# Performance work log

Hardware: AMD Instinct MI355X
Metric: run time of the kernel (lower is better)

Reference implementation:

```python
import jax, jax.numpy as jnp
import numpy as np

N = 100000
E = 1600000
IN = 256
H = 4
D = 32           # n_hidden per head
C = 47           # n_classes per head in last layer
NEG_SLOPE = 0.2


def setup_inputs() -> dict:
    key = jax.random.key(0)
    ks = jax.random.split(key, 20)
    x = jax.random.normal(ks[0], (N, IN), dtype=jnp.float32)
    src = jax.random.randint(ks[1], (E,), 0, N, dtype=jnp.int32)
    dst = jax.random.randint(ks[2], (E,), 0, N, dtype=jnp.int32)
    s = 0.05
    inp = {"x": x, "src": src, "dst": dst}
    # layer 0: in 256 -> (H=4, D=32)
    inp["W0s"] = jax.random.normal(ks[3], (IN, H * D), dtype=jnp.float32) * s
    inp["W0d"] = jax.random.normal(ks[4], (IN, H * D), dtype=jnp.float32) * s
    inp["a0l"] = jax.random.normal(ks[5], (H, D), dtype=jnp.float32) * s
    inp["a0r"] = jax.random.normal(ks[6], (H, D), dtype=jnp.float32) * s
    inp["b0"] = jnp.zeros((H, D), dtype=jnp.float32)
    # layer 1: in 128 -> (4, 32)
    inp["W1s"] = jax.random.normal(ks[7], (H * D, H * D), dtype=jnp.float32) * s
    inp["W1d"] = jax.random.normal(ks[8], (H * D, H * D), dtype=jnp.float32) * s
    inp["a1l"] = jax.random.normal(ks[9], (H, D), dtype=jnp.float32) * s
    inp["a1r"] = jax.random.normal(ks[10], (H, D), dtype=jnp.float32) * s
    inp["b1"] = jnp.zeros((H, D), dtype=jnp.float32)
    # layer 2: in 128 -> (4, 47), no activation
    inp["W2s"] = jax.random.normal(ks[11], (H * D, H * C), dtype=jnp.float32) * s
    inp["W2d"] = jax.random.normal(ks[12], (H * D, H * C), dtype=jnp.float32) * s
    inp["a2l"] = jax.random.normal(ks[13], (H, C), dtype=jnp.float32) * s
    inp["a2r"] = jax.random.normal(ks[14], (H, C), dtype=jnp.float32) * s
    inp["b2"] = jnp.zeros((H, C), dtype=jnp.float32)
    return inp


def _gat_layer(h, src, dst, Ws, Wd, al, ar, b):
    # h: [N, F_in]; full-graph block so h_dst == h
    n = h.shape[0]
    heads, dout = al.shape
    fs = (h @ Ws).reshape(n, heads, dout)   # [N, H, D]
    fd = (h @ Wd).reshape(n, heads, dout)
    el = jnp.sum(fs * al, axis=-1)          # [N, H]
    er = jnp.sum(fd * ar, axis=-1)
    e = el[src] + er[dst]                   # [E, H]
    e = jnp.where(e > 0, e, NEG_SLOPE * e)  # leaky_relu
    # segment softmax over incoming edges of each dst node
    m = jax.lax.stop_gradient(jax.ops.segment_max(e, dst, num_segments=n))
    ez = jnp.exp(e - m[dst])
    denom = jax.ops.segment_sum(ez, dst, num_segments=n)
    alpha = ez / denom[dst]                 # [E, H]
    msg = fs[src] * alpha[:, :, None]       # [E, H, D]
    rst = jax.ops.segment_sum(msg, dst, num_segments=n)  # [N, H, D]
    return rst + b


def reference(x, src, dst,
              W0s, W0d, a0l, a0r, b0,
              W1s, W1d, a1l, a1r, b1,
              W2s, W2d, a2l, a2r, b2):
    h = _gat_layer(x, src, dst, W0s, W0d, a0l, a0r, b0)
    h = jax.nn.relu(h).reshape(h.shape[0], -1)           # flatten(1)
    h = _gat_layer(h, src, dst, W1s, W1d, a1l, a1r, b1)
    h = jax.nn.relu(h).reshape(h.shape[0], -1)
    h = _gat_layer(h, src, dst, W2s, W2d, a2l, a2r, b2)  # [N, H, C]
    h = h.mean(axis=1)                                   # mean over heads
    return jax.nn.log_softmax(h, axis=-1)
```

## Files before the change

kernel.cpp:

```cpp
#include <hip/hip_runtime.h>
#include <math.h>

#define NEG_SLOPE 0.2f

typedef _Float16 half2v __attribute__((ext_vector_type(2)));
typedef _Float16 half8 __attribute__((ext_vector_type(8)));
typedef float float4v __attribute__((ext_vector_type(4)));
typedef float float2v __attribute__((ext_vector_type(2)));

__device__ __forceinline__ float lrelu(float x) { return x > 0.f ? x : NEG_SLOPE * x; }

__device__ __forceinline__ float sel4(const float4 v, int h) {
  float r = v.x;
  r = (h == 1) ? v.y : r;
  r = (h == 2) ? v.z : r;
  r = (h == 3) ? v.w : r;
  return r;
}

__device__ __forceinline__ unsigned char f32_to_fp8(float a) {
  int v = __builtin_amdgcn_cvt_pk_fp8_f32(a, 0.f, 0, false);
  return (unsigned char)(v & 0xff);
}


__global__ void k_hist(const int* __restrict__ dst, int* __restrict__ cnt, int E) {
  int i = blockIdx.x * blockDim.x + threadIdx.x;
  if (i < E) atomicAdd(&cnt[dst[i]], 1);
}

__global__ __launch_bounds__(256) void k_offsets(const int* __restrict__ cnt,
                                                 int* __restrict__ row_start,
                                                 int* __restrict__ gcount, int N) {
  __shared__ int s[256];
  __shared__ int base;
  int tid = threadIdx.x;
  int i = blockIdx.x * 256 + tid;
  int c = (i < N) ? cnt[i] : 0;
  s[tid] = c;
  __syncthreads();
  for (int off = 1; off < 256; off <<= 1) {
    int v = 0;
    if (tid >= off) v = s[tid - off];
    __syncthreads();
    if (tid >= off) s[tid] += v;
    __syncthreads();
  }
  if (tid == 255) base = atomicAdd(gcount, s[255]);
  __syncthreads();
  if (i < N) row_start[i] = base + s[tid] - c;
}

__global__ void k_scatter(const int* __restrict__ src, const int* __restrict__ dst,
                          const int* __restrict__ row_start, int* __restrict__ fill,
                          int* __restrict__ srcs, int E) {
  int i = blockIdx.x * blockDim.x + threadIdx.x;
  if (i < E) {
    int d = dst[i];
    int p = row_start[d] + atomicAdd(&fill[d], 1);
    srcs[p] = src[i];
  }
}

__device__ __forceinline__ void wlr_one(const float* Ws, const float* Wd,
                                        const float* al, const float* ar,
                                        float* wlr, int K, int Dh, int i) {
  int M = 4 * Dh;
  int k = i >> 2, h = i & 3;
  float sl = 0.f, sr = 0.f;
  for (int d = 0; d < Dh; d++) {
    sl += Ws[(size_t)k * M + h * Dh + d] * al[h * Dh + d];
    sr += Wd[(size_t)k * M + h * Dh + d] * ar[h * Dh + d];
  }
  wlr[k * 8 + h] = sl;
  wlr[k * 8 + 4 + h] = sr;
}

__global__ __launch_bounds__(256) void k_prep(
    const float* __restrict__ W0s, const float* __restrict__ W0d,
    const float* __restrict__ a0l, const float* __restrict__ a0r,
    const float* __restrict__ W1s, const float* __restrict__ W1d,
    const float* __restrict__ a1l, const float* __restrict__ a1r,
    const float* __restrict__ W2s, const float* __restrict__ W2d,
    const float* __restrict__ a2l, const float* __restrict__ a2r,
    float* __restrict__ wlr0, float* __restrict__ wlr1, float* __restrict__ wlr2,
    _Float16* __restrict__ Wt0, _Float16* __restrict__ Wt1, _Float16* __restrict__ Wt2) {
  int i = blockIdx.x * 256 + threadIdx.x;
  if (i < 1024) {
    wlr_one(W0s, W0d, a0l, a0r, wlr0, 256, 32, i);
  } else if (i < 1536) {
    wlr_one(W1s, W1d, a1l, a1r, wlr1, 128, 32, i - 1024);
  } else if (i < 2048) {
    wlr_one(W2s, W2d, a2l, a2r, wlr2, 128, 47, i - 1536);
  } else if (i < 2048 + 32768) {
    int j = i - 2048;
    int m = j >> 8, k = j & 255;
    Wt0[j] = (_Float16)W0s[(size_t)k * 128 + m];
  } else if (i < 2048 + 32768 + 16384) {
    int j = i - (2048 + 32768);
    int m = j >> 7, k = j & 127;
    Wt1[j] = (_Float16)W1s[(size_t)k * 128 + m];
  } else if (i < 2048 + 32768 + 16384 + 24576) {
    int j = i - (2048 + 32768 + 16384);
    int r = j >> 7, k = j & 127;
    int h = r / 48, c = r % 48;
    float v = (c < 47) ? W2s[(size_t)k * 188 + 47 * h + c] : 0.f;
    Wt2[j] = (_Float16)v;
  }
}

template <int BN, typename AT>
__global__ __launch_bounds__(256) void k_gemm_mfma(const AT* __restrict__ A,
                                                   const _Float16* __restrict__ Bt,
                                                   const float* __restrict__ wlr,
                                                   unsigned char* __restrict__ C,
                                                   float* __restrict__ el,
                                                   float* __restrict__ er, int N, int K) {
  constexpr int NT = BN / 64;
  constexpr int ASZ = 4 * 64 * 8;
  constexpr int BSZ = (BN / 16) * 64 * 8;
  constexpr int SSZ = ASZ + BSZ;
  __shared__ __align__(16) _Float16 smem[SSZ];
  __shared__ float swlr[2048];
  _Float16* As = smem;
  _Float16* Bs = smem + ASZ;

  const int tid = threadIdx.x;
  const int lane = tid & 63;
  const int w = tid >> 6;
  const int row0 = blockIdx.x * 64;

  for (int i = tid; i < K * 8; i += 256) swlr[i] = wlr[i];
  __syncthreads();

  float4v acc[4][NT];
#pragma unroll
  for (int i = 0; i < 4; i++)
#pragma unroll
    for (int j = 0; j < NT; j++) acc[i][j] = (float4v){0.f, 0.f, 0.f, 0.f};
  float p[8] = {0, 0, 0, 0, 0, 0, 0, 0};

  const int ar_ = tid >> 2, aq = tid & 3;
  for (int k0 = 0; k0 < K; k0 += 32) {
    {
      int gr = row0 + ar_;
      float a8[8];
      if (gr < N) {
        if constexpr (sizeof(AT) == 4) {
          const float4* pp = (const float4*)&A[(size_t)gr * K + k0 + aq * 8];
          float4 u0 = pp[0], u1 = pp[1];
          a8[0] = u0.x; a8[1] = u0.y; a8[2] = u0.z; a8[3] = u0.w;
          a8[4] = u1.x; a8[5] = u1.y; a8[6] = u1.z; a8[7] = u1.w;
        } else {
          half8 hv = *(const half8*)&A[(size_t)gr * K + k0 + aq * 8];
#pragma unroll
          for (int j = 0; j < 8; j++) a8[j] = (float)hv[j];
        }
      } else {
#pragma unroll
        for (int j = 0; j < 8; j++) a8[j] = 0.f;
      }
      half8 v;
#pragma unroll
      for (int j = 0; j < 8; j++) v[j] = (_Float16)a8[j];
      *(half8*)&As[(size_t)(((ar_ >> 4) * 64) + (ar_ & 15) + 16 * aq) * 8] = v;
#pragma unroll
      for (int j = 0; j < 8; j++) {
        const float av = a8[j];
        const float* wp = &swlr[(k0 + aq * 8 + j) * 8];
        float4 w0 = *(const float4*)wp;
        float4 w1 = *(const float4*)(wp + 4);
        p[0] += av * w0.x; p[1] += av * w0.y; p[2] += av * w0.z; p[3] += av * w0.w;
        p[4] += av * w1.x; p[5] += av * w1.y; p[6] += av * w1.z; p[7] += av * w1.w;
      }
    }
#pragma unroll
    for (int i = 0; i < NT; i++) {
      int idx = tid + i * 256;
      int n = idx >> 2, q = idx & 3;
      half8 v = *(const half8*)&Bt[(size_t)n * K + k0 + q * 8];
      *(half8*)&Bs[(size_t)((n >> 4) * 64 + (n & 15) + 16 * q) * 8] = v;
    }
    __syncthreads();
    half8 af[4];
#pragma unroll
    for (int mt = 0; mt < 4; mt++) af[mt] = *(half8*)&As[(size_t)(mt * 64 + lane) * 8];
#pragma unroll
    for (int nt = 0; nt < NT; nt++) {
      half8 bf = *(half8*)&Bs[(size_t)((w * NT + nt) * 64 + lane) * 8];
#pragma unroll
      for (int mt = 0; mt < 4; mt++)
        acc[mt][nt] = __builtin_amdgcn_mfma_f32_16x16x32_f16(af[mt], bf, acc[mt][nt], 0, 0, 0);
    }
    __syncthreads();
  }

#pragma unroll
  for (int j = 0; j < 8; j++) swlr[(ar_ * 4 + aq) * 8 + j] = p[j];

  unsigned char* cs = (unsigned char*)smem;
  const int quad = lane >> 4;
#pragma unroll
  for (int mt = 0; mt < 4; mt++)
#pragma unroll
    for (int nt = 0; nt < NT; nt++)
#pragma unroll
      for (int reg = 0; reg < 4; reg++) {
        int r = mt * 16 + quad * 4 + reg;
        int cc = (w * NT + nt) * 16 + (lane & 15);
        cs[r * BN + cc] = f32_to_fp8(acc[mt][nt][reg]);
      }
  __syncthreads();
  if (tid < 64) {
    int gr = row0 + tid;
    if (gr < N) {
      float e[8];
#pragma unroll
      for (int j = 0; j < 8; j++)
        e[j] = swlr[(tid * 4 + 0) * 8 + j] + swlr[(tid * 4 + 1) * 8 + j] +
               swlr[(tid * 4 + 2) * 8 + j] + swlr[(tid * 4 + 3) * 8 + j];
      *(float4*)&el[(size_t)gr * 4] = make_float4(e[0], e[1], e[2], e[3]);
      *(float4*)&er[(size_t)gr * 4] = make_float4(e[4], e[5], e[6], e[7]);
    }
  }
  constexpr int PER = (64 * BN) / (256 * 16);
  const uint4* s4 = (const uint4*)cs;
#pragma unroll
  for (int i = 0; i < PER; i++) {
    int idx = tid + i * 256;
    int r = idx / (BN / 16), c16 = idx % (BN / 16);
    int gr = row0 + r;
    if (gr < N) *(uint4*)&C[(size_t)gr * BN + c16 * 16] = s4[idx];
  }
}

__global__ __launch_bounds__(256) void k_edge_mid(
    const unsigned char* __restrict__ F, const float* __restrict__ el,
    const float* __restrict__ er, const int* __restrict__ row_start,
    const int* __restrict__ cnt, const int* __restrict__ srcs,
    const float* __restrict__ bias, _Float16* __restrict__ hout, int N) {
  __shared__ float sEz[4][64][4];
  __shared__ int sU[4][64];
  int lane = threadIdx.x & 63;
  int w = threadIdx.x >> 6;
  int v = blockIdx.x * 4 + w;
  if (v >= N) return;
  int start = row_start[v], deg = cnt[v];
  float4 erv = *(const float4*)&er[(size_t)v * 4];
  const int g = lane >> 4;
  const int fl = lane & 15;
  const int h = fl >> 2;
  float acc[8] = {0, 0, 0, 0, 0, 0, 0, 0};
  float4 lsum = make_float4(0.f, 0.f, 0.f, 0.f);

  for (int c = 0; c < deg; c += 64) {
    int take = min(64, deg - c);
    if (lane < take) {
      int u = srcs[start + c + lane];
      float4 e = *(const float4*)&el[(size_t)u * 4];
      float4 ez;
      ez.x = __expf(lrelu(e.x + erv.x));
      ez.y = __expf(lrelu(e.y + erv.y));
      ez.z = __expf(lrelu(e.z + erv.z));
      ez.w = __expf(lrelu(e.w + erv.w));
      lsum.x += ez.x; lsum.y += ez.y; lsum.z += ez.z; lsum.w += ez.w;
      sU[w][lane] = u;
      *(float4*)&sEz[w][lane][0] = ez;
    }
    for (int kk = g; kk < take; kk += 4) {
      int u = sU[w][kk];
      float ezh = sEz[w][kk][h];
      uint2 d = *(const uint2*)&F[(size_t)u * 128 + 8 * fl];
      float2v c0 = __builtin_amdgcn_cvt_pk_f32_fp8((int)d.x, false);
      float2v c1 = __builtin_amdgcn_cvt_pk_f32_fp8((int)d.x, true);
      float2v c2 = __builtin_amdgcn_cvt_pk_f32_fp8((int)d.y, false);
      float2v c3 = __builtin_amdgcn_cvt_pk_f32_fp8((int)d.y, true);
      acc[0] += ezh * c0.x; acc[1] += ezh * c0.y;
      acc[2] += ezh * c1.x; acc[3] += ezh * c1.y;
      acc[4] += ezh * c2.x; acc[5] += ezh * c2.y;
      acc[6] += ezh * c3.x; acc[7] += ezh * c3.y;
    }
  }
#pragma unroll
  for (int j = 0; j < 8; j++) {
    acc[j] += __shfl_xor(acc[j], 16);
    acc[j] += __shfl_xor(acc[j], 32);
  }
#pragma unroll
  for (int msk = 1; msk < 64; msk <<= 1) {
    lsum.x += __shfl_xor(lsum.x, msk);
    lsum.y += __shfl_xor(lsum.y, msk);
    lsum.z += __shfl_xor(lsum.z, msk);
    lsum.w += __shfl_xor(lsum.w, msk);
  }
  if (g == 0) {
    float inv = (deg > 0) ? 1.f / sel4(lsum, h) : 0.f;
    const float4* bp = (const float4*)&bias[8 * fl];
    float4 b0v = bp[0], b1v = bp[1];
    float bb[8] = {b0v.x, b0v.y, b0v.z, b0v.w, b1v.x, b1v.y, b1v.z, b1v.w};
    half8 o;
#pragma unroll
    for (int j = 0; j < 8; j++) o[j] = (_Float16)fmaxf(fmaf(acc[j], inv, bb[j]), 0.f);
    *(half8*)&hout[(size_t)v * 128 + 8 * fl] = o;
  }
}

__global__ __launch_bounds__(256) void k_edge_final(
    const unsigned char* __restrict__ F, const float* __restrict__ el,
    const float* __restrict__ er, const int* __restrict__ row_start,
    const int* __restrict__ cnt, const int* __restrict__ srcs,
    const float* __restrict__ b2, float* __restrict__ out, int N) {
  __shared__ float sEz[4][64][4];
  __shared__ int sU[4][64];
  __shared__ float red[4][192];
  int lane = threadIdx.x & 63;
  int w = threadIdx.x >> 6;
  int v = blockIdx.x * 4 + w;
  if (v >= N) return;
  int start = row_start[v], deg = cnt[v];
  float4 erv = *(const float4*)&er[(size_t)v * 4];
  const int sub = lane >> 5;
  const int l24 = lane & 31;
  const bool act = l24 < 24;
  const int h = l24 / 6;
  const int j6 = l24 % 6;
  const int foff = 48 * h + 8 * j6;
  float acc[8] = {0, 0, 0, 0, 0, 0, 0, 0};
  float4 lsum = make_float4(0.f, 0.f, 0.f, 0.f);

  for (int c = 0; c < deg; c += 64) {
    int take = min(64, deg - c);
    if (lane < take) {
      int u = srcs[start + c + lane];
      float4 e = *(const float4*)&el[(size_t)u * 4];
      float4 ez;
      ez.x = __expf(lrelu(e.x + erv.x));
      ez.y = __expf(lrelu(e.y + erv.y));
      ez.z = __expf(lrelu(e.z + erv.z));
      ez.w = __expf(lrelu(e.w + erv.w));
      lsum.x += ez.x; lsum.y += ez.y; lsum.z += ez.z; lsum.w += ez.w;
      sU[w][lane] = u;
      *(float4*)&sEz[w][lane][0] = ez;
    }
    if (act) {
      for (int kk = sub; kk < take; kk += 2) {
        int u = sU[w][kk];
        float ezh = sEz[w][kk][h];
        uint2 d = *(const uint2*)&F[(size_t)u * 192 + foff];
        float2v c0 = __builtin_amdgcn_cvt_pk_f32_fp8((int)d.x, false);
        float2v c1 = __builtin_amdgcn_cvt_pk_f32_fp8((int)d.x, true);
        float2v c2 = __builtin_amdgcn_cvt_pk_f32_fp8((int)d.y, false);
        float2v c3 = __builtin_amdgcn_cvt_pk_f32_fp8((int)d.y, true);
        acc[0] += ezh * c0.x; acc[1] += ezh * c0.y;
        acc[2] += ezh * c1.x; acc[3] += ezh * c1.y;
        acc[4] += ezh * c2.x; acc[5] += ezh * c2.y;
        acc[6] += ezh * c3.x; acc[7] += ezh * c3.y;
      }
    }
  }
#pragma unroll
  for (int j = 0; j < 8; j++) acc[j] += __shfl_xor(acc[j], 32);
#pragma unroll
  for (int msk = 1; msk < 64; msk <<= 1) {
    lsum.x += __shfl_xor(lsum.x, msk);
    lsum.y += __shfl_xor(lsum.y, msk);
    lsum.z += __shfl_xor(lsum.z, msk);
    lsum.w += __shfl_xor(lsum.w, msk);
  }
  if (act && sub == 0) {
    float inv = (deg > 0) ? 1.f / sel4(lsum, h) : 0.f;
#pragma unroll
    for (int j = 0; j < 8; j++) {
      int cc = 8 * j6 + j;
      float bv = (cc < 47) ? b2[47 * h + cc] : 0.f;
      red[w][foff + j] = fmaf(acc[j], inv, bv);
    }
  }
  __syncthreads();
  float g = -INFINITY;
  if (lane < 47)
    g = 0.25f * (red[w][lane] + red[w][lane + 48] + red[w][lane + 96] + red[w][lane + 144]);
  float gm = g;
#pragma unroll
  for (int msk = 1; msk < 64; msk <<= 1) gm = fmaxf(gm, __shfl_xor(gm, msk));
  float ex = (lane < 47) ? __expf(g - gm) : 0.f;
  float s = ex;
#pragma unroll
  for (int msk = 1; msk < 64; msk <<= 1) s += __shfl_xor(s, msk);
  if (lane < 47) out[(size_t)v * 47 + lane] = g - gm - __logf(s);
}

extern "C" void kernel_launch(void* const* d_in, const int* in_sizes, int n_in,
                              void* d_out, int out_size, void* d_ws, size_t ws_size,
                              hipStream_t stream) {
  const float* x = (const float*)d_in[0];
  const int* src = (const int*)d_in[1];
  const int* dst = (const int*)d_in[2];
  const float* W0s = (const float*)d_in[3];
  const float* W0d = (const float*)d_in[4];
  const float* a0l = (const float*)d_in[5];
  const float* a0r = (const float*)d_in[6];
  const float* b0 = (const float*)d_in[7];
  const float* W1s = (const float*)d_in[8];
  const float* W1d = (const float*)d_in[9];
  const float* a1l = (const float*)d_in[10];
  const float* a1r = (const float*)d_in[11];
  const float* b1 = (const float*)d_in[12];
  const float* W2s = (const float*)d_in[13];
  const float* W2d = (const float*)d_in[14];
  const float* a2l = (const float*)d_in[15];
  const float* a2r = (const float*)d_in[16];
  const float* b2 = (const float*)d_in[17];
  float* out = (float*)d_out;

  const int N = in_sizes[0] / 256;
  const int E = in_sizes[1];

  char* w = (char*)d_ws;
  size_t off = 0;
  auto alloc = [&](size_t bytes) -> void* {
    void* p = w + off;
    off += (bytes + 255) & ~(size_t)255;
    return p;
  };
  int* gcount = (int*)alloc(4);
  int* cnt = (int*)alloc((size_t)N * 4);
  int* fill = (int*)alloc((size_t)N * 4);
  size_t zbytes = off;
  int* row_start = (int*)alloc((size_t)N * 4);
  int* srcs = (int*)alloc((size_t)E * 4);
  float* wlr0 = (float*)alloc(256 * 8 * 4);
  float* wlr1 = (float*)alloc(128 * 8 * 4);
  float* wlr2 = (float*)alloc(128 * 8 * 4);
  _Float16* Wt0 = (_Float16*)alloc(128 * 256 * 2);
  _Float16* Wt1 = (_Float16*)alloc(128 * 128 * 2);
  _Float16* Wt2 = (_Float16*)alloc(192 * 128 * 2);
  float* el = (float*)alloc((size_t)N * 4 * 4);
  float* er = (float*)alloc((size_t)N * 4 * 4);
  unsigned char* F = (unsigned char*)alloc((size_t)N * 192);
  _Float16* Ha = (_Float16*)alloc((size_t)N * 128 * 2);
  _Float16* Hc = (_Float16*)alloc((size_t)N * 128 * 2);
  (void)ws_size;

  hipMemsetAsync(d_ws, 0, zbytes, stream);
  k_hist<<<(E + 255) / 256, 256, 0, stream>>>(dst, cnt, E);
  k_offsets<<<(N + 255) / 256, 256, 0, stream>>>(cnt, row_start, gcount, N);
  k_scatter<<<(E + 255) / 256, 256, 0, stream>>>(src, dst, row_start, fill, srcs, E);
  k_prep<<<(75776 + 255) / 256, 256, 0, stream>>>(W0s, W0d, a0l, a0r, W1s, W1d, a1l, a1r,
                                                  W2s, W2d, a2l, a2r, wlr0, wlr1, wlr2,
                                                  Wt0, Wt1, Wt2);

  int gemm_grid = (N + 63) / 64;
  int node_grid = (N + 3) / 4;

  k_gemm_mfma<128, float><<<gemm_grid, 256, 0, stream>>>(x, Wt0, wlr0, F, el, er, N, 256);
  k_edge_mid<<<node_grid, 256, 0, stream>>>(F, el, er, row_start, cnt, srcs, b0, Ha, N);

  k_gemm_mfma<128, _Float16><<<gemm_grid, 256, 0, stream>>>(Ha, Wt1, wlr1, F, el, er, N, 128);
  k_edge_mid<<<node_grid, 256, 0, stream>>>(F, el, er, row_start, cnt, srcs, b1, Hc, N);

  k_gemm_mfma<192, _Float16><<<gemm_grid, 256, 0, stream>>>(Hc, Wt2, wlr2, F, el, er, N, 128);
  k_edge_final<<<node_grid, 256, 0, stream>>>(F, el, er, row_start, cnt, srcs, b2, out, N);
}
```

Before: 680.1 us.

## Split attention-logit and edge-exp computation into separate kernels before aggregation

Removes the el/er dot-product computation from the MFMA GEMM and moves it to a dedicated per-node kernel that rereads the layer input. A new per-edge kernel precomputes exp(leaky_relu(el[src]+er[dst])) into a CSR-ordered buffer, using a new dsts array written during scatter. The aggregation kernels then stream srcs and Ez with software prefetch instead of staging through shared memory, and the final layer uses 16-byte feature loads. This simplifies the GEMM and aggregation loops but adds extra global traffic: the input features are reread and an E×4 float buffer is written and read per layer, plus extra launches.

```diff
diff --git a/kernel.cpp b/kernel.cpp
--- a/kernel.cpp
+++ b/kernel.cpp
@@ -3,24 +3,31 @@
 
 #define NEG_SLOPE 0.2f
 
-typedef _Float16 half2v __attribute__((ext_vector_type(2)));
 typedef _Float16 half8 __attribute__((ext_vector_type(8)));
 typedef float float4v __attribute__((ext_vector_type(4)));
 typedef float float2v __attribute__((ext_vector_type(2)));
 
 __device__ __forceinline__ float lrelu(float x) { return x > 0.f ? x : NEG_SLOPE * x; }
 
-__device__ __forceinline__ float sel4(const float4 v, int h) {
-  float r = v.x;
-  r = (h == 1) ? v.y : r;
-  r = (h == 2) ? v.z : r;
-  r = (h == 3) ? v.w : r;
-  return r;
-}
-
 __device__ __forceinline__ unsigned char f32_to_fp8(float a) {
   int v = __builtin_amdgcn_cvt_pk_fp8_f32(a, 0.f, 0, false);
   return (unsigned char)(v & 0xff);
+}
+
+__device__ __forceinline__ void acc_fp8x8(float* acc, uint2 d, float ez) {
+  float2v c0 = __builtin_amdgcn_cvt_pk_f32_fp8((int)d.x, false);
+  float2v c1 = __builtin_amdgcn_cvt_pk_f32_fp8((int)d.x, true);
+  float2v c2 = __builtin_amdgcn_cvt_pk_f32_fp8((int)d.y, false);
+  float2v c3 = __builtin_amdgcn_cvt_pk_f32_fp8((int)d.y, true);
+  acc[0] += ez * c0.x; acc[1] += ez * c0.y;
+  acc[2] += ez * c1.x; acc[3] += ez * c1.y;
+  acc[4] += ez * c2.x; acc[5] += ez * c2.y;
+  acc[6] += ez * c3.x; acc[7] += ez * c3.y;
+}
+
+__device__ __forceinline__ void acc_fp8x16(float* acc, uint4 d, float ez) {
+  acc_fp8x8(acc, make_uint2(d.x, d.y), ez);
+  acc_fp8x8(acc + 8, make_uint2(d.z, d.w), ez);
 }
 
 
@@ -53,12 +60,13 @@
 
 __global__ void k_scatter(const int* __restrict__ src, const int* __restrict__ dst,
                           const int* __restrict__ row_start, int* __restrict__ fill,
-                          int* __restrict__ srcs, int E) {
+                          int* __restrict__ srcs, int* __restrict__ dsts, int E) {
   int i = blockIdx.x * blockDim.x + threadIdx.x;
   if (i < E) {
     int d = dst[i];
     int p = row_start[d] + atomicAdd(&fill[d], 1);
     srcs[p] = src[i];
+    dsts[p] = d;
   }
 }
 
@@ -109,19 +117,62 @@
   }
 }
 
+template <typename T>
+__global__ __launch_bounds__(256) void k_eler(const T* __restrict__ H,
+                                              const float* __restrict__ wlr,
+                                              float* __restrict__ el, float* __restrict__ er,
+                                              int N, int K) {
+  __shared__ float ws[2048];
+  for (int i = threadIdx.x; i < K * 8; i += 256) ws[i] = wlr[i];
+  __syncthreads();
+  int lane = threadIdx.x & 63;
+  int node = blockIdx.x * 4 + (threadIdx.x >> 6);
+  if (node >= N) return;
+  float p[8] = {0, 0, 0, 0, 0, 0, 0, 0};
+  for (int k = lane; k < K; k += 64) {
+    float hv = (float)H[(size_t)node * K + k];
+#pragma unroll
+    for (int j = 0; j < 8; j++) p[j] += hv * ws[k * 8 + j];
+  }
+#pragma unroll
+  for (int j = 0; j < 8; j++) {
+#pragma unroll
+    for (int m = 1; m < 64; m <<= 1) p[j] += __shfl_xor(p[j], m);
+  }
+  if (lane == 0) {
+    *(float4*)&el[(size_t)node * 4] = make_float4(p[0], p[1], p[2], p[3]);
+    *(float4*)&er[(size_t)node * 4] = make_float4(p[4], p[5], p[6], p[7]);
+  }
+}
+
+__global__ __launch_bounds__(256) void k_ez(const int* __restrict__ srcs,
+                                            const int* __restrict__ dsts,
+                                            const float* __restrict__ el,
+                                            const float* __restrict__ er,
+                                            float* __restrict__ Ez, int E) {
+  int p = blockIdx.x * 256 + threadIdx.x;
+  if (p < E) {
+    int u = srcs[p], d = dsts[p];
+    float4 a = *(const float4*)&el[(size_t)u * 4];
+    float4 b = *(const float4*)&er[(size_t)d * 4];
+    float4 z;
+    z.x = __expf(lrelu(a.x + b.x));
+    z.y = __expf(lrelu(a.y + b.y));
+    z.z = __expf(lrelu(a.z + b.z));
+    z.w = __expf(lrelu(a.w + b.w));
+    *(float4*)&Ez[(size_t)p * 4] = z;
+  }
+}
+
 template <int BN, typename AT>
 __global__ __launch_bounds__(256) void k_gemm_mfma(const AT* __restrict__ A,
                                                    const _Float16* __restrict__ Bt,
-                                                   const float* __restrict__ wlr,
-                                                   unsigned char* __restrict__ C,
-                                                   float* __restrict__ el,
-                                                   float* __restrict__ er, int N, int K) {
+                                                   unsigned char* __restrict__ C, int N, int K) {
   constexpr int NT = BN / 64;
   constexpr int ASZ = 4 * 64 * 8;
   constexpr int BSZ = (BN / 16) * 64 * 8;
   constexpr int SSZ = ASZ + BSZ;
   __shared__ __align__(16) _Float16 smem[SSZ];
-  __shared__ float swlr[2048];
   _Float16* As = smem;
   _Float16* Bs = smem + ASZ;
 
@@ -130,49 +181,31 @@
   const int w = tid >> 6;
   const int row0 = blockIdx.x * 64;
 
-  for (int i = tid; i < K * 8; i += 256) swlr[i] = wlr[i];
-  __syncthreads();
-
   float4v acc[4][NT];
 #pragma unroll
   for (int i = 0; i < 4; i++)
 #pragma unroll
     for (int j = 0; j < NT; j++) acc[i][j] = (float4v){0.f, 0.f, 0.f, 0.f};
-  float p[8] = {0, 0, 0, 0, 0, 0, 0, 0};
 
   const int ar_ = tid >> 2, aq = tid & 3;
   for (int k0 = 0; k0 < K; k0 += 32) {
     {
       int gr = row0 + ar_;
-      float a8[8];
+      half8 v;
       if (gr < N) {
         if constexpr (sizeof(AT) == 4) {
           const float4* pp = (const float4*)&A[(size_t)gr * K + k0 + aq * 8];
           float4 u0 = pp[0], u1 = pp[1];
-          a8[0] = u0.x; a8[1] = u0.y; a8[2] = u0.z; a8[3] = u0.w;
-          a8[4] = u1.x; a8[5] = u1.y; a8[6] = u1.z; a8[7] = u1.w;
+          v[0] = (_Float16)u0.x; v[1] = (_Float16)u0.y; v[2] = (_Float16)u0.z; v[3] = (_Float16)u0.w;
+          v[4] = (_Float16)u1.x; v[5] = (_Float16)u1.y; v[6] = (_Float16)u1.z; v[7] = (_Float16)u1.w;
         } else {
-          half8 hv = *(const half8*)&A[(size_t)gr * K + k0 + aq * 8];
-#pragma unroll
-          for (int j = 0; j < 8; j++) a8[j] = (float)hv[j];
+          v = *(const half8*)&A[(size_t)gr * K + k0 + aq * 8];
         }
       } else {
 #pragma unroll
-        for (int j = 0; j < 8; j++) a8[j] = 0.f;
+        for (int j = 0; j < 8; j++) v[j] = (_Float16)0.f;
       }
-      half8 v;
-#pragma unroll
-      for (int j = 0; j < 8; j++) v[j] = (_Float16)a8[j];
       *(half8*)&As[(size_t)(((ar_ >> 4) * 64) + (ar_ & 15) + 16 * aq) * 8] = v;
-#pragma unroll
-      for (int j = 0; j < 8; j++) {
-        const float av = a8[j];
-        const float* wp = &swlr[(k0 + aq * 8 + j) * 8];
-        float4 w0 = *(const float4*)wp;
-        float4 w1 = *(const float4*)(wp + 4);
-        p[0] += av * w0.x; p[1] += av * w0.y; p[2] += av * w0.z; p[3] += av * w0.w;
-        p[4] += av * w1.x; p[5] += av * w1.y; p[6] += av * w1.z; p[7] += av * w1.w;
-      }
     }
 #pragma unroll
     for (int i = 0; i < NT; i++) {
@@ -194,9 +227,6 @@
     }
     __syncthreads();
   }
-
-#pragma unroll
-  for (int j = 0; j < 8; j++) swlr[(ar_ * 4 + aq) * 8 + j] = p[j];
 
   unsigned char* cs = (unsigned char*)smem;
   const int quad = lane >> 4;
@@ -211,18 +241,6 @@
         cs[r * BN + cc] = f32_to_fp8(acc[mt][nt][reg]);
       }
   __syncthreads();
-  if (tid < 64) {
-    int gr = row0 + tid;
-    if (gr < N) {
-      float e[8];
-#pragma unroll
-      for (int j = 0; j < 8; j++)
-        e[j] = swlr[(tid * 4 + 0) * 8 + j] + swlr[(tid * 4 + 1) * 8 + j] +
-               swlr[(tid * 4 + 2) * 8 + j] + swlr[(tid * 4 + 3) * 8 + j];
-      *(float4*)&el[(size_t)gr * 4] = make_float4(e[0], e[1], e[2], e[3]);
-      *(float4*)&er[(size_t)gr * 4] = make_float4(e[4], e[5], e[6], e[7]);
-    }
-  }
   constexpr int PER = (64 * BN) / (256 * 16);
   const uint4* s4 = (const uint4*)cs;
 #pragma unroll
@@ -234,67 +252,51 @@
   }
 }
 
-__global__ __launch_bounds__(256) void k_edge_mid(
-    const unsigned char* __restrict__ F, const float* __restrict__ el,
-    const float* __restrict__ er, const int* __restrict__ row_start,
-    const int* __restrict__ cnt, const int* __restrict__ srcs,
-    const float* __restrict__ bias, _Float16* __restrict__ hout, int N) {
-  __shared__ float sEz[4][64][4];
-  __shared__ int sU[4][64];
+__global__ __launch_bounds__(256) void k_agg_mid(
+    const unsigned char* __restrict__ F, const float* __restrict__ Ez,
+    const int* __restrict__ row_start, const int* __restrict__ cnt,
+    const int* __restrict__ srcs, const float* __restrict__ bias,
+    _Float16* __restrict__ hout, int N) {
   int lane = threadIdx.x & 63;
-  int w = threadIdx.x >> 6;
-  int v = blockIdx.x * 4 + w;
+  int v = blockIdx.x * 4 + (threadIdx.x >> 6);
   if (v >= N) return;
   int start = row_start[v], deg = cnt[v];
-  float4 erv = *(const float4*)&er[(size_t)v * 4];
+  int end = start + deg;
   const int g = lane >> 4;
   const int fl = lane & 15;
   const int h = fl >> 2;
   float acc[8] = {0, 0, 0, 0, 0, 0, 0, 0};
-  float4 lsum = make_float4(0.f, 0.f, 0.f, 0.f);
-
-  for (int c = 0; c < deg; c += 64) {
-    int take = min(64, deg - c);
-    if (lane < take) {
-      int u = srcs[start + c + lane];
-      float4 e = *(const float4*)&el[(size_t)u * 4];
-      float4 ez;
-      ez.x = __expf(lrelu(e.x + erv.x));
-      ez.y = __expf(lrelu(e.y + erv.y));
-      ez.z = __expf(lrelu(e.z + erv.z));
-      ez.w = __expf(lrelu(e.w + erv.w));
-      lsum.x += ez.x; lsum.y += ez.y; lsum.z += ez.z; lsum.w += ez.w;
-      sU[w][lane] = u;
-      *(float4*)&sEz[w][lane][0] = ez;
-    }
-    for (int kk = g; kk < take; kk += 4) {
-      int u = sU[w][kk];
-      float ezh = sEz[w][kk][h];
-      uint2 d = *(const uint2*)&F[(size_t)u * 128 + 8 * fl];
-      float2v c0 = __builtin_amdgcn_cvt_pk_f32_fp8((int)d.x, false);
-      float2v c1 = __builtin_amdgcn_cvt_pk_f32_fp8((int)d.x, true);
-      float2v c2 = __builtin_amdgcn_cvt_pk_f32_fp8((int)d.y, false);
-      float2v c3 = __builtin_amdgcn_cvt_pk_f32_fp8((int)d.y, true);
-      acc[0] += ezh * c0.x; acc[1] += ezh * c0.y;
-      acc[2] += ezh * c1.x; acc[3] += ezh * c1.y;
-      acc[4] += ezh * c2.x; acc[5] += ezh * c2.y;
-      acc[6] += ezh * c3.x; acc[7] += ezh * c3.y;
-    }
+  float lsum = 0.f;
+
+  int pg = start + g;
+  int u = 0;
+  float ezv = 0.f;
+  if (pg < end) {
+    u = srcs[pg];
+    ezv = Ez[(size_t)pg * 4 + h];
+  }
+  while (pg < end) {
+    int pn = pg + 4;
+    int u2 = 0;
+    float ez2 = 0.f;
+    if (pn < end) {
+      u2 = srcs[pn];
+      ez2 = Ez[(size_t)pn * 4 + h];
+    }
+    uint2 d = *(const uint2*)&F[(size_t)u * 128 + 8 * fl];
+    acc_fp8x8(acc, d, ezv);
+    lsum += ezv;
+    u = u2; ezv = ez2; pg = pn;
   }
 #pragma unroll
   for (int j = 0; j < 8; j++) {
     acc[j] += __shfl_xor(acc[j], 16);
     acc[j] += __shfl_xor(acc[j], 32);
   }
-#pragma unroll
-  for (int msk = 1; msk < 64; msk <<= 1) {
-    lsum.x += __shfl_xor(lsum.x, msk);
-    lsum.y += __shfl_xor(lsum.y, msk);
-    lsum.z += __shfl_xor(lsum.z, msk);
-    lsum.w += __shfl_xor(lsum.w, msk);
-  }
+  lsum += __shfl_xor(lsum, 16);
+  lsum += __shfl_xor(lsum, 32);
   if (g == 0) {
-    float inv = (deg > 0) ? 1.f / sel4(lsum, h) : 0.f;
+    float inv = (deg > 0) ? 1.f / lsum : 0.f;
     const float4* bp = (const float4*)&bias[8 * fl];
     float4 b0v = bp[0], b1v = bp[1];
     float bb[8] = {b0v.x, b0v.y, b0v.z, b0v.w, b1v.x, b1v.y, b1v.z, b1v.w};
@@ -305,89 +307,78 @@
   }
 }
 
-__global__ __launch_bounds__(256) void k_edge_final(
-    const unsigned char* __restrict__ F, const float* __restrict__ el,
-    const float* __restrict__ er, const int* __restrict__ row_start,
-    const int* __restrict__ cnt, const int* __restrict__ srcs,
-    const float* __restrict__ b2, float* __restrict__ out, int N) {
-  __shared__ float sEz[4][64][4];
-  __shared__ int sU[4][64];
+__global__ __launch_bounds__(256) void k_agg_final(
+    const unsigned char* __restrict__ F, const float* __restrict__ Ez,
+    const int* __restrict__ row_start, const int* __restrict__ cnt,
+    const int* __restrict__ srcs, const float* __restrict__ b2,
+    float* __restrict__ out, int N) {
   __shared__ float red[4][192];
   int lane = threadIdx.x & 63;
   int w = threadIdx.x >> 6;
   int v = blockIdx.x * 4 + w;
   if (v >= N) return;
   int start = row_start[v], deg = cnt[v];
-  float4 erv = *(const float4*)&er[(size_t)v * 4];
-  const int sub = lane >> 5;
-  const int l24 = lane & 31;
-  const bool act = l24 < 24;
-  const int h = l24 / 6;
-  const int j6 = l24 % 6;
-  const int foff = 48 * h + 8 * j6;
-  float acc[8] = {0, 0, 0, 0, 0, 0, 0, 0};
-  float4 lsum = make_float4(0.f, 0.f, 0.f, 0.f);
-
-  for (int c = 0; c < deg; c += 64) {
-    int take = min(64, deg - c);
-    if (lane < take) {
-      int u = srcs[start + c + lane];
-      float4 e = *(const float4*)&el[(size_t)u * 4];
-      float4 ez;
-      ez.x = __expf(lrelu(e.x + erv.x));
-      ez.y = __expf(lrelu(e.y + erv.y));
-      ez.z = __expf(lrelu(e.z + erv.z));
-      ez.w = __expf(lrelu(e.w + erv.w));
-      lsum.x += ez.x; lsum.y += ez.y; lsum.z += ez.z; lsum.w += ez.w;
-      sU[w][lane] = u;
-      *(float4*)&sEz[w][lane][0] = ez;
-    }
-    if (act) {
-      for (int kk = sub; kk < take; kk += 2) {
-        int u = sU[w][kk];
-        float ezh = sEz[w][kk][h];
-        uint2 d = *(const uint2*)&F[(size_t)u * 192 + foff];
-        float2v c0 = __builtin_amdgcn_cvt_pk_f32_fp8((int)d.x, false);
-        float2v c1 = __builtin_amdgcn_cvt_pk_f32_fp8((int)d.x, true);
-        float2v c2 = __builtin_amdgcn_cvt_pk_f32_fp8((int)d.y, false);
-        float2v c3 = __builtin_amdgcn_cvt_pk_f32_fp8((int)d.y, true);
-        acc[0] += ezh * c0.x; acc[1] += ezh * c0.y;
-        acc[2] += ezh * c1.x; acc[3] += ezh * c1.y;
-        acc[4] += ezh * c2.x; acc[5] += ezh * c2.y;
-        acc[6] += ezh * c3.x; acc[7] += ezh * c3.y;
+  int end = start + deg;
+  const int g = lane >> 4;
+  const int fl = lane & 15;
+  const bool act = fl < 12;
+  const int h = fl / 3;
+  float acc[16];
+#pragma unroll
+  for (int j = 0; j < 16; j++) acc[j] = 0.f;
+  float lsum = 0.f;
+
+  if (act) {
+    int pg = start + g;
+    int u = 0;
+    float ezv = 0.f;
+    if (pg < end) {
+      u = srcs[pg];
+      ezv = Ez[(size_t)pg * 4 + h];
+    }
+    while (pg < end) {
+      int pn = pg + 4;
+      int u2 = 0;
+      float ez2 = 0.f;
+      if (pn < end) {
+        u2 = srcs[pn];
+        ez2 = Ez[(size_t)pn * 4 + h];
       }
-    }
-  }
-#pragma unroll
-  for (int j = 0; j < 8; j++) acc[j] += __shfl_xor(acc[j], 32);
-#pragma unroll
-  for (int msk = 1; msk < 64; msk <<= 1) {
-    lsum.x += __shfl_xor(lsum.x, msk);
-    lsum.y += __shfl_xor(lsum.y, msk);
-    lsum.z += __shfl_xor(lsum.z, msk);
-    lsum.w += __shfl_xor(lsum.w, msk);
-  }
-  if (act && sub == 0) {
-    float inv = (deg > 0) ? 1.f / sel4(lsum, h) : 0.f;
-#pragma unroll
-    for (int j = 0; j < 8; j++) {
-      int cc = 8 * j6 + j;
-      float bv = (cc < 47) ? b2[47 * h + cc] : 0.f;
-      red[w][foff + j] = fmaf(acc[j], inv, bv);
+      uint4 d = *(const uint4*)&F[(size_t)u * 192 + 16 * fl];
+      acc_fp8x16(acc, d, ezv);
+      lsum += ezv;
+      u = u2; ezv = ez2; pg = pn;
+    }
+  }
+#pragma unroll
+  for (int j = 0; j < 16; j++) {
+    acc[j] += __shfl_xor(acc[j], 16);
+    acc[j] += __shfl_xor(acc[j], 32);
+  }
+  lsum += __shfl_xor(lsum, 16);
+  lsum += __shfl_xor(lsum, 32);
+  if (g == 0 && act) {
+    float inv = (deg > 0) ? 1.f / lsum : 0.f;
+    int c0 = 16 * (fl % 3);
+#pragma unroll
+    for (int j = 0; j < 16; j++) {
+      int c = c0 + j;
+      float bv = (c < 47) ? b2[47 * h + c] : 0.f;
+      red[w][16 * fl + j] = fmaf(acc[j], inv, bv);
     }
   }
   __syncthreads();
-  float g = -INFINITY;
+  float gg = -INFINITY;
   if (lane < 47)
-    g = 0.25f * (red[w][lane] + red[w][lane + 48] + red[w][lane + 96] + red[w][lane + 144]);
-  float gm = g;
+    gg = 0.25f * (red[w][lane] + red[w][lane + 48] + red[w][lane + 96] + red[w][lane + 144]);
+  float gm = gg;
 #pragma unroll
   for (int msk = 1; msk < 64; msk <<= 1) gm = fmaxf(gm, __shfl_xor(gm, msk));
-  float ex = (lane < 47) ? __expf(g - gm) : 0.f;
+  float ex = (lane < 47) ? __expf(gg - gm) : 0.f;
   float s = ex;
 #pragma unroll
   for (int msk = 1; msk < 64; msk <<= 1) s += __shfl_xor(s, msk);
-  if (lane < 47) out[(size_t)v * 47 + lane] = g - gm - __logf(s);
+  if (lane < 47) out[(size_t)v * 47 + lane] = gg - gm - __logf(s);
 }
 
 extern "C" void kernel_launch(void* const* d_in, const int* in_sizes, int n_in,
@@ -429,6 +420,8 @@
   size_t zbytes = off;
   int* row_start = (int*)alloc((size_t)N * 4);
   int* srcs = (int*)alloc((size_t)E * 4);
+  int* dsts = (int*)alloc((size_t)E * 4);
+  float* Ez = (float*)alloc((size_t)E * 4 * 4);
   float* wlr0 = (float*)alloc(256 * 8 * 4);
   float* wlr1 = (float*)alloc(128 * 8 * 4);
   float* wlr2 = (float*)alloc(128 * 8 * 4);
@@ -445,20 +438,27 @@
   hipMemsetAsync(d_ws, 0, zbytes, stream);
   k_hist<<<(E + 255) / 256, 256, 0, stream>>>(dst, cnt, E);
   k_offsets<<<(N + 255) / 256, 256, 0, stream>>>(cnt, row_start, gcount, N);
-  k_scatter<<<(E + 255) / 256, 256, 0, stream>>>(src, dst, row_start, fill, srcs, E);
+  k_scatter<<<(E + 255) / 256, 256, 0, stream>>>(src, dst, row_start, fill, srcs, dsts, E);
   k_prep<<<(75776 + 255) / 256, 256, 0, stream>>>(W0s, W0d, a0l, a0r, W1s, W1d, a1l, a1r,
                                                   W2s, W2d, a2l, a2r, wlr0, wlr1, wlr2,
                                                   Wt0, Wt1, Wt2);
 
   int gemm_grid = (N + 63) / 64;
   int node_grid = (N + 3) / 4;
-
-  k_gemm_mfma<128, float><<<gemm_grid, 256, 0, stream>>>(x, Wt0, wlr0, F, el, er, N, 256);
-  k_edge_mid<<<node_grid, 256, 0, stream>>>(F, el, er, row_start, cnt, srcs, b0, Ha, N);
-
-  k_gemm_mfma<128, _Float16><<<gemm_grid, 256, 0, stream>>>(Ha, Wt1, wlr1, F, el, er, N, 128);
-  k_edge_mid<<<node_grid, 256, 0, stream>>>(F, el, er, row_start, cnt, srcs, b1, Hc, N);
-
-  k_gemm_mfma<192, _Float16><<<gemm_grid, 256, 0, stream>>>(Hc, Wt2, wlr2, F, el, er, N, 128);
-  k_edge_final<<<node_grid, 256, 0, stream>>>(F, el, er, row_start, cnt, srcs, b2, out, N);
-}
+  int edge_grid = (E + 255) / 256;
+
+  k_gemm_mfma<128, float><<<gemm_grid, 256, 0, stream>>>(x, Wt0, F, N, 256);
+  k_eler<float><<<node_grid, 256, 0, stream>>>(x, wlr0, el, er, N, 256);
+  k_ez<<<edge_grid, 256, 0, stream>>>(srcs, dsts, el, er, Ez, E);
+  k_agg_mid<<<node_grid, 256, 0, stream>>>(F, Ez, row_start, cnt, srcs, b0, Ha, N);
+
+  k_gemm_mfma<128, _Float16><<<gemm_grid, 256, 0, stream>>>(Ha, Wt1, F, N, 128);
+  k_eler<_Float16><<<node_grid, 256, 0, stream>>>(Ha, wlr1, el, er, N, 128);
+  k_ez<<<edge_grid, 256, 0, stream>>>(srcs, dsts, el, er, Ez, E);
+  k_agg_mid<<<node_grid, 256, 0, stream>>>(F, Ez, row_start, cnt, srcs, b1, Hc, N);
+
+  k_gemm_mfma<192, _Float16><<<gemm_grid, 256, 0, stream>>>(Hc, Wt2, F, N, 128);
+  k_eler<_Float16><<<node_grid, 256, 0, stream>>>(Hc, wlr2, el, er, N, 128);
+  k_ez<<<edge_grid, 256, 0, stream>>>(srcs, dsts, el, er, Ez, E);
+  k_agg_final<<<node_grid, 256, 0, stream>>>(F, Ez, row_start, cnt, srcs, b2, out, N);
+}
```

New measurement: 864.2 us. 1.27x slower.
